# Optimization experiments

Measured on AMD Instinct MI355X. Metric: run time of the kernel, lower is better.

The kernel has to match this reference:

```python
import jax, jax.numpy as jnp
import numpy as np

K = 20
ALPHA = 0.2  # leaky relu slope


def knn_idx(x, k):
    # x: [B, C, N]. Negative squared pairwise distance, top-k neighbors.
    inner = -2.0 * jnp.einsum('bcn,bcm->bnm', x, x)           # [B,N,N]
    xx = jnp.sum(x * x, axis=1)                                # [B,N]
    neg_dist = -xx[:, :, None] - inner - xx[:, None, :]        # [B,N,N]
    _, idx = jax.lax.top_k(neg_dist, k)                        # [B,N,k]
    return idx


def setup_inputs() -> dict:
    key = jax.random.key(0)
    k1, k2, k3 = jax.random.split(key, 3)
    B, C, N = 8, 64, 2048
    out_ch = 64
    x = jax.random.normal(k1, (B, C, N), dtype=jnp.float32)
    W = jax.random.normal(k2, (out_ch, 2 * C), dtype=jnp.float32) * (1.0 / np.sqrt(2 * C))
    b = jax.random.normal(k3, (out_ch,), dtype=jnp.float32) * 0.01
    return {"x": x, "W": W, "b": b}


def reference(x, W, b):
    # x: [B,C,N], W: [O,2C] (1x1 conv weight), b: [O]
    idx = knn_idx(x, K)                                        # [B,N,k] int32
    xt = jnp.transpose(x, (0, 2, 1))                           # [B,N,C]
    gather = jax.vmap(lambda xb, ib: xb[ib])                   # per-batch gather
    feat = gather(xt, idx)                                     # [B,N,k,C]
    center = xt[:, :, None, :]                                 # [B,N,1,C]
    # concat(neighbor - center, center) -> [B,N,k,2C]
    edge = jnp.concatenate([feat - center, jnp.broadcast_to(center, feat.shape)], axis=-1)
    # 1x1 conv over channels == matmul on last dim, then leaky relu
    h = jnp.einsum('bnkc,oc->bonk', edge, W) + b[None, :, None, None]  # [B,O,N,k]
    h = jnp.where(h >= 0, h, ALPHA * h)
    # max aggregation over neighbor axis
    return jnp.max(h, axis=-1)                                 # [B,O,N]
```

## Files before the change

### kernel.cpp

```cpp
#include <hip/hip_runtime.h>
#include <math.h>

#define BATCH 8
#define CH    64
#define NPTS  2048
#define KNN   20
#define OUTC  64

__device__ __forceinline__ void ladder20(float (&d)[KNN], int (&id)[KNN], float iv, int ii) {
    bool ci = true;
    #pragma unroll
    for (int s = 0; s < KNN; ++s) {
        const bool  cn = (s < KNN-1) ? (iv > d[s+1]) : false;
        const float dn = (s < KNN-1) ? d[s+1] : 0.f;
        const int   gn = (s < KNN-1) ? id[s+1] : 0;
        d[s]  = cn ? dn : (ci ? iv : d[s]);
        id[s] = cn ? gn : (ci ? ii : id[s]);
        ci = cn;
    }
}

__global__ __launch_bounds__(256) void edgeconv_prep(
    const float* __restrict__ x, const float* __restrict__ W,
    const float* __restrict__ bias,
    float* __restrict__ y1t, float* __restrict__ zt, float* __restrict__ xx)
{
    __shared__ __align__(16) float Wt1[64*65];
    __shared__ __align__(16) float Wtd[64*65];
    __shared__ __align__(16) float xs [64*32];
    const int tx  = threadIdx.x;
    const int bid = blockIdx.x;
    const int b   = bid >> 6;
    const int m0  = (bid & 63) << 5;
    const float* xb = x + (size_t)b * (CH * NPTS);

    {
        const int o  = tx >> 2;
        const int cb = (tx & 3) << 4;
        #pragma unroll
        for (int cc = 0; cc < 16; cc += 4) {
            const float4 w1 = *(const float4*)&W[o*128 + cb + cc];
            const float4 w2 = *(const float4*)&W[o*128 + 64 + cb + cc];
            const float a1[4] = {w1.x, w1.y, w1.z, w1.w};
            const float a2[4] = {w2.x, w2.y, w2.z, w2.w};
            #pragma unroll
            for (int e = 0; e < 4; ++e) {
                Wt1[(cb+cc+e)*65 + o] = a1[e];
                Wtd[(cb+cc+e)*65 + o] = a2[e] - a1[e];
            }
        }
    }
    {
        const int c0 = tx >> 2;
        const int j0 = (tx & 3) << 3;
        *(float4*)&xs[c0*32 + j0]     = *(const float4*)&xb[(size_t)c0*NPTS + m0 + j0];
        *(float4*)&xs[c0*32 + j0 + 4] = *(const float4*)&xb[(size_t)c0*NPTS + m0 + j0 + 4];
    }
    __syncthreads();

    if (tx < 32) {
        float s = 0.f;
        #pragma unroll
        for (int c = 0; c < 64; ++c) { const float v = xs[c*32 + tx]; s = fmaf(v, v, s); }
        xx[b*NPTS + m0 + tx] = s;
    }

    const int o  = tx & 63;
    const int mg = tx >> 6;
    float y[8], z[8];
    const float bo = bias[o];
    #pragma unroll
    for (int i = 0; i < 8; ++i) { y[i] = 0.f; z[i] = bo; }
    #pragma unroll 8
    for (int c = 0; c < 64; ++c) {
        const float w1 = Wt1[c*65 + o];
        const float wd = Wtd[c*65 + o];
        float a[8];
        *(float4*)&a[0] = *(const float4*)&xs[c*32 + mg*8];
        *(float4*)&a[4] = *(const float4*)&xs[c*32 + mg*8 + 4];
        #pragma unroll
        for (int i = 0; i < 8; ++i) {
            y[i] = fmaf(w1, a[i], y[i]);
            z[i] = fmaf(wd, a[i], z[i]);
        }
    }
    #pragma unroll
    for (int i = 0; i < 8; ++i) {
        const int m = m0 + mg*8 + i;
        y1t[((size_t)b*NPTS + m)*64 + o] = y[i];
        zt [((size_t)b*NPTS + m)*64 + o] = z[i];
    }
}

__global__ __launch_bounds__(256) void edgeconv_main(
    const float* __restrict__ x,
    const float* __restrict__ y1t, const float* __restrict__ zt,
    const float* __restrict__ xx, float* __restrict__ out)
{
    __shared__ __align__(16) char pool[43520];
    float* xnt = (float*)pool;
    float* xmb = (float*)(pool + 8704);
    float* xxb = (float*)(pool + 41472);
    float* mv  = (float*)pool;
    int*   mi  = (int*)(pool + 20480);
    int*   ml  = (int*)(pool + 40960);
    float* outbuf = (float*)pool;

    const int tx  = threadIdx.x;
    const int bid = blockIdx.x;
    const int b   = bid >> 6;
    const int n0  = (bid & 63) << 5;
    const float* xb = x + (size_t)b * (CH * NPTS);

    {
        const int rr = tx >> 3;
        const int c8 = (tx & 7) << 3;
        #pragma unroll
        for (int i = 0; i < 8; ++i)
            xnt[rr*68 + c8 + i] = xb[(size_t)(c8 + i)*NPTS + n0 + rr];
    }
    {
        const int c = tx >> 4;
        const int j = (tx & 15) << 2;
        #pragma unroll
        for (int it = 0; it < 4; ++it)
            *(float4*)&xmb[(c + it*16)*64 + j] = *(const float4*)&xb[(size_t)(c + it*16)*NPTS + j];
        if (tx < 64) xxb[tx] = xx[b*NPTS + tx];
    }

    const int r = tx >> 3;
    const int q = tx & 7;
    float d[KNN]; int id[KNN];
    #pragma unroll
    for (int k = 0; k < KNN; ++k) { d[k] = -INFINITY; id[k] = 0; }
    float thrR = -INFINITY;

    for (int t = 0; t < 32; ++t) {
        __syncthreads();
        const int cur = t & 1;
        const float* bufc = xmb + cur*4096;
        const float* xxc  = xxb + cur*64;
        float* bufn = xmb + (cur^1)*4096;
        float* xxn  = xxb + (cur^1)*64;

        float4 p0, p1, p2, p3;
        float xxp = 0.f;
        const int tn  = t + 1;
        const int jj  = (tx & 15) << 2;
        const int cc4 = tx >> 4;
        if (tn < 32) {
            const int mb2 = tn << 6;
            p0 = *(const float4*)&xb[(size_t)(cc4 +  0)*NPTS + mb2 + jj];
            p1 = *(const float4*)&xb[(size_t)(cc4 + 16)*NPTS + mb2 + jj];
            p2 = *(const float4*)&xb[(size_t)(cc4 + 32)*NPTS + mb2 + jj];
            p3 = *(const float4*)&xb[(size_t)(cc4 + 48)*NPTS + mb2 + jj];
            if (tx < 64) xxp = xx[b*NPTS + mb2 + tx];
        }

        float acc8[8];
        #pragma unroll
        for (int e = 0; e < 8; ++e) acc8[e] = 0.f;
        #pragma unroll 4
        for (int c4 = 0; c4 < 64; c4 += 4) {
            float av[4];
            *(float4*)&av[0] = *(const float4*)&xnt[r*68 + c4];
            #pragma unroll
            for (int i = 0; i < 4; ++i) {
                float bv[8];
                *(float4*)&bv[0] = *(const float4*)&bufc[(c4+i)*64 + q*4];
                *(float4*)&bv[4] = *(const float4*)&bufc[(c4+i)*64 + q*4 + 32];
                #pragma unroll
                for (int e = 0; e < 8; ++e) acc8[e] = fmaf(av[i], bv[e], acc8[e]);
            }
        }

        float xq[8];
        *(float4*)&xq[0] = *(const float4*)&xxc[q*4];
        *(float4*)&xq[4] = *(const float4*)&xxc[q*4 + 32];
        float v[8];
        unsigned msk = 0u;
        #pragma unroll
        for (int e = 0; e < 8; ++e) {
            v[e] = fmaf(2.f, acc8[e], -xq[e]);
            msk |= (v[e] > thrR) ? (1u << e) : 0u;
        }

        const int base = (t << 6) + (q << 2);
        while (__any(msk != 0u)) {
            const bool act = (msk != 0u);
            const int  e   = __ffs(msk) - 1;
            msk &= msk - 1u;
            const float t01 = (e & 1) ? v[1] : v[0];
            const float t23 = (e & 1) ? v[3] : v[2];
            const float t45 = (e & 1) ? v[5] : v[4];
            const float t67 = (e & 1) ? v[7] : v[6];
            const float t03 = (e & 2) ? t23 : t01;
            const float t47 = (e & 2) ? t67 : t45;
            const float vv  = (e & 4) ? t47 : t03;
            if (act && vv > d[0]) ladder20(d, id, vv, base + (e & 3) + ((e & 4) ? 32 : 0));
        }

        float tm = d[0];
        tm = fmaxf(tm, __shfl_xor(tm, 1));
        tm = fmaxf(tm, __shfl_xor(tm, 2));
        tm = fmaxf(tm, __shfl_xor(tm, 4));
        thrR = tm;

        if (tn < 32) {
            *(float4*)&bufn[(cc4 +  0)*64 + jj] = p0;
            *(float4*)&bufn[(cc4 + 16)*64 + jj] = p1;
            *(float4*)&bufn[(cc4 + 32)*64 + jj] = p2;
            *(float4*)&bufn[(cc4 + 48)*64 + jj] = p3;
            if (tx < 64) xxn[tx] = xxp;
        }
    }
    __syncthreads();

    #pragma unroll
    for (int k = 0; k < KNN; ++k) { mv[tx*20 + k] = d[k]; mi[tx*20 + k] = id[k]; }
    __syncthreads();

    if (q == 0) {
        float hv[8]; int hi[8]; int hp[8];
        #pragma unroll
        for (int s = 0; s < 8; ++s) {
            hp[s] = KNN - 1;
            hv[s] = mv[(r*8 + s)*20 + KNN - 1];
            hi[s] = mi[(r*8 + s)*20 + KNN - 1];
        }
        for (int k = 0; k < KNN; ++k) {
            float bv = hv[0]; int bg = hi[0]; int bs = 0;
            #pragma unroll
            for (int s = 1; s < 8; ++s) {
                const bool better = (hv[s] > bv) || (hv[s] == bv && hi[s] < bg);
                bv = better ? hv[s] : bv;
                bg = better ? hi[s] : bg;
                bs = better ? s : bs;
            }
            ml[r*20 + k] = bg;
            #pragma unroll
            for (int s = 0; s < 8; ++s) {
                if (bs == s) {
                    const int np  = hp[s] - 1;
                    hp[s] = np;
                    const bool ok = (np >= 0);
                    const int npc = ok ? np : 0;
                    const float nv = mv[(r*8 + s)*20 + npc];
                    const int   ng = mi[(r*8 + s)*20 + npc];
                    hv[s] = ok ? nv : -INFINITY;
                    hi[s] = ok ? ng : 0;
                }
            }
        }
    }
    __syncthreads();

    const int lane = tx & 63;
    const int w    = tx >> 6;
    const float* y1b = y1t + (size_t)b * NPTS * 64;
    const float* ztb = zt  + (size_t)b * NPTS * 64;

    for (int rr = 0; rr < 8; ++rr) {
        const int rw = w*8 + rr;
        const int n  = n0 + rw;
        const float zv = ztb[(size_t)n*64 + lane];
        float acc = -INFINITY;
        #pragma unroll
        for (int k = 0; k < KNN; ++k) {
            const int m = ml[rw*20 + k];
            const float vv = y1b[(size_t)m*64 + lane];
            float h = vv + zv;
            h = fmaxf(h, 0.2f*h);
            acc = fmaxf(acc, h);
        }
        outbuf[rw*68 + lane] = acc;
    }
    __syncthreads();
    float* ob = out + (size_t)b * OUTC * NPTS;
    #pragma unroll
    for (int qo = 0; qo < 8; ++qo) {
        const int o = w*16 + qo*2 + (lane >> 5);
        const int n = lane & 31;
        ob[(size_t)o*NPTS + n0 + n] = outbuf[n*68 + o];
    }
}

extern "C" void kernel_launch(void* const* d_in, const int* in_sizes, int n_in,
                              void* d_out, int out_size, void* d_ws, size_t ws_size,
                              hipStream_t stream) {
    const float* x    = (const float*)d_in[0];
    const float* W    = (const float*)d_in[1];
    const float* bias = (const float*)d_in[2];
    float* out = (float*)d_out;

    float* y1t = (float*)d_ws;
    float* zt  = y1t + (size_t)BATCH * NPTS * 64;
    float* xx  = zt  + (size_t)BATCH * NPTS * 64;

    edgeconv_prep<<<BATCH * (NPTS/32), 256, 0, stream>>>(x, W, bias, y1t, zt, xx);
    edgeconv_main<<<BATCH * (NPTS/32), 256, 0, stream>>>(x, y1t, zt, xx, out);
}
```

Measured before the change: 307.0 us.

## Halve query points per block, use 16 lanes per row with shuffle-based top-k merge

Each block of edgeconv_main now handles 16 query points instead of 32, with 16 threads per query each scanning 4 candidates per tile, so the grid doubles to 1024 blocks. The final merge of per-thread top-20 lists moves from a shared-memory 8-way merge done by one thread per row to a 20-round wave-shuffle argmax across the 16 lanes. The xx values are kept in registers instead of shared memory, which shrinks LDS use. The cost is that the candidate tile is re-read from global memory by twice as many blocks, and the per-lane register top-k lists gain more total ladder insertions.

```diff
diff --git a/kernel.cpp b/kernel.cpp
--- a/kernel.cpp
+++ b/kernel.cpp
@@ -97,27 +97,27 @@
     const float* __restrict__ y1t, const float* __restrict__ zt,
     const float* __restrict__ xx, float* __restrict__ out)
 {
-    __shared__ __align__(16) char pool[43520];
+    __shared__ __align__(16) char pool[37120];
     float* xnt = (float*)pool;
-    float* xmb = (float*)(pool + 8704);
-    float* xxb = (float*)(pool + 41472);
-    float* mv  = (float*)pool;
-    int*   mi  = (int*)(pool + 20480);
-    int*   ml  = (int*)(pool + 40960);
-    float* outbuf = (float*)pool;
+    float* xmb = (float*)(pool + 4352);
+    int*   ml     = (int*)pool;
+    float* outbuf = (float*)(pool + 1280);
 
     const int tx  = threadIdx.x;
     const int bid = blockIdx.x;
-    const int b   = bid >> 6;
-    const int n0  = (bid & 63) << 5;
-    const float* xb = x + (size_t)b * (CH * NPTS);
-
-    {
-        const int rr = tx >> 3;
-        const int c8 = (tx & 7) << 3;
-        #pragma unroll
-        for (int i = 0; i < 8; ++i)
-            xnt[rr*68 + c8 + i] = xb[(size_t)(c8 + i)*NPTS + n0 + rr];
+    const int b   = bid >> 7;
+    const int n0  = (bid & 127) << 4;
+    const float* xb   = x  + (size_t)b * (CH * NPTS);
+    const float* xxbg = xx + (size_t)b * NPTS;
+
+    const int r = tx >> 4;
+    const int q = tx & 15;
+
+    {
+        const int c4b = q << 2;
+        #pragma unroll
+        for (int i = 0; i < 4; ++i)
+            xnt[r*68 + c4b + i] = xb[(size_t)(c4b + i)*NPTS + n0 + r];
     }
     {
         const int c = tx >> 4;
@@ -125,11 +125,11 @@
         #pragma unroll
         for (int it = 0; it < 4; ++it)
             *(float4*)&xmb[(c + it*16)*64 + j] = *(const float4*)&xb[(size_t)(c + it*16)*NPTS + j];
-        if (tx < 64) xxb[tx] = xx[b*NPTS + tx];
-    }
-
-    const int r = tx >> 3;
-    const int q = tx & 7;
+    }
+
+    float xq[4];
+    *(float4*)&xq[0] = *(const float4*)&xxbg[q*4];
+
     float d[KNN]; int id[KNN];
     #pragma unroll
     for (int k = 0; k < KNN; ++k) { d[k] = -INFINITY; id[k] = 0; }
@@ -139,12 +139,9 @@
         __syncthreads();
         const int cur = t & 1;
         const float* bufc = xmb + cur*4096;
-        const float* xxc  = xxb + cur*64;
         float* bufn = xmb + (cur^1)*4096;
-        float* xxn  = xxb + (cur^1)*64;
-
-        float4 p0, p1, p2, p3;
-        float xxp = 0.f;
+
+        float4 p0, p1, p2, p3, xqn;
         const int tn  = t + 1;
         const int jj  = (tx & 15) << 2;
         const int cc4 = tx >> 4;
@@ -154,34 +151,30 @@
             p1 = *(const float4*)&xb[(size_t)(cc4 + 16)*NPTS + mb2 + jj];
             p2 = *(const float4*)&xb[(size_t)(cc4 + 32)*NPTS + mb2 + jj];
             p3 = *(const float4*)&xb[(size_t)(cc4 + 48)*NPTS + mb2 + jj];
-            if (tx < 64) xxp = xx[b*NPTS + mb2 + tx];
-        }
-
-        float acc8[8];
-        #pragma unroll
-        for (int e = 0; e < 8; ++e) acc8[e] = 0.f;
-        #pragma unroll 4
+            xqn = *(const float4*)&xxbg[mb2 + (q << 2)];
+        }
+
+        float acc[4];
+        #pragma unroll
+        for (int e = 0; e < 4; ++e) acc[e] = 0.f;
+        #pragma unroll
         for (int c4 = 0; c4 < 64; c4 += 4) {
             float av[4];
             *(float4*)&av[0] = *(const float4*)&xnt[r*68 + c4];
             #pragma unroll
             for (int i = 0; i < 4; ++i) {
-                float bv[8];
-                *(float4*)&bv[0] = *(const float4*)&bufc[(c4+i)*64 + q*4];
-                *(float4*)&bv[4] = *(const float4*)&bufc[(c4+i)*64 + q*4 + 32];
+                float bv[4];
+                *(float4*)&bv[0] = *(const float4*)&bufc[(c4+i)*64 + (q << 2)];
                 #pragma unroll
-                for (int e = 0; e < 8; ++e) acc8[e] = fmaf(av[i], bv[e], acc8[e]);
+                for (int e = 0; e < 4; ++e) acc[e] = fmaf(av[i], bv[e], acc[e]);
             }
         }
 
-        float xq[8];
-        *(float4*)&xq[0] = *(const float4*)&xxc[q*4];
-        *(float4*)&xq[4] = *(const float4*)&xxc[q*4 + 32];
-        float v[8];
+        float v[4];
         unsigned msk = 0u;
         #pragma unroll
-        for (int e = 0; e < 8; ++e) {
-            v[e] = fmaf(2.f, acc8[e], -xq[e]);
+        for (int e = 0; e < 4; ++e) {
+            v[e] = fmaf(2.f, acc[e], -xq[e]);
             msk |= (v[e] > thrR) ? (1u << e) : 0u;
         }
 
@@ -192,18 +185,15 @@
             msk &= msk - 1u;
             const float t01 = (e & 1) ? v[1] : v[0];
             const float t23 = (e & 1) ? v[3] : v[2];
-            const float t45 = (e & 1) ? v[5] : v[4];
-            const float t67 = (e & 1) ? v[7] : v[6];
-            const float t03 = (e & 2) ? t23 : t01;
-            const float t47 = (e & 2) ? t67 : t45;
-            const float vv  = (e & 4) ? t47 : t03;
-            if (act && vv > d[0]) ladder20(d, id, vv, base + (e & 3) + ((e & 4) ? 32 : 0));
+            const float vv  = (e & 2) ? t23 : t01;
+            if (act && vv > d[0]) ladder20(d, id, vv, base + e);
         }
 
         float tm = d[0];
         tm = fmaxf(tm, __shfl_xor(tm, 1));
         tm = fmaxf(tm, __shfl_xor(tm, 2));
         tm = fmaxf(tm, __shfl_xor(tm, 4));
+        tm = fmaxf(tm, __shfl_xor(tm, 8));
         thrR = tm;
 
         if (tn < 32) {
@@ -211,46 +201,24 @@
             *(float4*)&bufn[(cc4 + 16)*64 + jj] = p1;
             *(float4*)&bufn[(cc4 + 32)*64 + jj] = p2;
             *(float4*)&bufn[(cc4 + 48)*64 + jj] = p3;
-            if (tx < 64) xxn[tx] = xxp;
-        }
-    }
-    __syncthreads();
-
-    #pragma unroll
-    for (int k = 0; k < KNN; ++k) { mv[tx*20 + k] = d[k]; mi[tx*20 + k] = id[k]; }
-    __syncthreads();
-
-    if (q == 0) {
-        float hv[8]; int hi[8]; int hp[8];
-        #pragma unroll
-        for (int s = 0; s < 8; ++s) {
-            hp[s] = KNN - 1;
-            hv[s] = mv[(r*8 + s)*20 + KNN - 1];
-            hi[s] = mi[(r*8 + s)*20 + KNN - 1];
-        }
-        for (int k = 0; k < KNN; ++k) {
-            float bv = hv[0]; int bg = hi[0]; int bs = 0;
+            *(float4*)&xq[0] = xqn;
+        }
+    }
+    __syncthreads();
+
+    for (int k = 0; k < KNN; ++k) {
+        float bv = d[KNN-1]; int bg = id[KNN-1];
+        #pragma unroll
+        for (int m = 1; m <= 8; m <<= 1) {
+            const float ov = __shfl_xor(bv, m);
+            const int   og = __shfl_xor(bg, m);
+            if (ov > bv || (ov == bv && og < bg)) { bv = ov; bg = og; }
+        }
+        if (q == 0) ml[r*20 + k] = bg;
+        if (d[KNN-1] == bv && id[KNN-1] == bg) {
             #pragma unroll
-            for (int s = 1; s < 8; ++s) {
-                const bool better = (hv[s] > bv) || (hv[s] == bv && hi[s] < bg);
-                bv = better ? hv[s] : bv;
-                bg = better ? hi[s] : bg;
-                bs = better ? s : bs;
-            }
-            ml[r*20 + k] = bg;
-            #pragma unroll
-            for (int s = 0; s < 8; ++s) {
-                if (bs == s) {
-                    const int np  = hp[s] - 1;
-                    hp[s] = np;
-                    const bool ok = (np >= 0);
-                    const int npc = ok ? np : 0;
-                    const float nv = mv[(r*8 + s)*20 + npc];
-                    const int   ng = mi[(r*8 + s)*20 + npc];
-                    hv[s] = ok ? nv : -INFINITY;
-                    hi[s] = ok ? ng : 0;
-                }
-            }
+            for (int s = KNN-1; s > 0; --s) { d[s] = d[s-1]; id[s] = id[s-1]; }
+            d[0] = -INFINITY; id[0] = 0;
         }
     }
     __syncthreads();
@@ -260,8 +228,9 @@
     const float* y1b = y1t + (size_t)b * NPTS * 64;
     const float* ztb = zt  + (size_t)b * NPTS * 64;
 
-    for (int rr = 0; rr < 8; ++rr) {
-        const int rw = w*8 + rr;
+    #pragma unroll
+    for (int rr = 0; rr < 4; ++rr) {
+        const int rw = w*4 + rr;
         const int n  = n0 + rw;
         const float zv = ztb[(size_t)n*64 + lane];
         float acc = -INFINITY;
@@ -278,9 +247,9 @@
     __syncthreads();
     float* ob = out + (size_t)b * OUTC * NPTS;
     #pragma unroll
-    for (int qo = 0; qo < 8; ++qo) {
-        const int o = w*16 + qo*2 + (lane >> 5);
-        const int n = lane & 31;
+    for (int qo = 0; qo < 4; ++qo) {
+        const int o = w*16 + qo*4 + (lane >> 4);
+        const int n = lane & 15;
         ob[(size_t)o*NPTS + n0 + n] = outbuf[n*68 + o];
     }
 }
@@ -298,5 +267,5 @@
     float* xx  = zt  + (size_t)BATCH * NPTS * 64;
 
     edgeconv_prep<<<BATCH * (NPTS/32), 256, 0, stream>>>(x, W, bias, y1t, zt, xx);
-    edgeconv_main<<<BATCH * (NPTS/32), 256, 0, stream>>>(x, y1t, zt, xx, out);
-}
+    edgeconv_main<<<BATCH * (NPTS/16), 256, 0, stream>>>(x, y1t, zt, xx, out);
+}
```

Result: slower. 340.1 us (+10.8%).
